# Kernel optimization log

Measured on AMD Instinct MI355X. Metric: run time of the kernel, lower is better.

Reference implementation:

```python
import jax, jax.numpy as jnp
import numpy as np

B, T, D, DH, DFF = 4, 2048, 1024, 1024, 4096


def setup_inputs() -> dict:
    key = jax.random.key(0)
    ks = jax.random.split(key, 8)
    s = 0.02
    return {
        "x": jax.random.normal(ks[0], (B, T, D), jnp.float32),
        "ln1_g": jnp.ones((D,), jnp.float32),
        "ln1_b": jnp.zeros((D,), jnp.float32),
        "W_q": jax.random.normal(ks[1], (D, DH), jnp.float32) * s,
        "b_q": jnp.zeros((DH,), jnp.float32),
        "W_k": jax.random.normal(ks[2], (D, DH), jnp.float32) * s,
        "b_k": jnp.zeros((DH,), jnp.float32),
        "W_v": jax.random.normal(ks[3], (D, DH), jnp.float32) * s,
        "b_v": jnp.zeros((DH,), jnp.float32),
        "ln2_g": jnp.ones((D,), jnp.float32),
        "ln2_b": jnp.zeros((D,), jnp.float32),
        "W_in": jax.random.normal(ks[4], (D, DFF), jnp.float32) * s,
        "b_in": jnp.zeros((DFF,), jnp.float32),
        "W_out": jax.random.normal(ks[5], (DFF, D), jnp.float32) * s,
        "b_out": jnp.zeros((D,), jnp.float32),
    }


def _layernorm(x, g, b, eps=1e-5):
    mu = jnp.mean(x, axis=-1, keepdims=True)
    var = jnp.var(x, axis=-1, keepdims=True)
    return (x - mu) * jax.lax.rsqrt(var + eps) * g + b


def reference(x, ln1_g, ln1_b, W_q, b_q, W_k, b_k, W_v, b_v,
              ln2_g, ln2_b, W_in, b_in, W_out, b_out):
    # --- attention branch (pre-LN) ---
    h = _layernorm(x, ln1_g, ln1_b)                      # [B,T,D]
    Q = h @ W_q + b_q                                    # [B,T,DH]
    K = h @ W_k + b_k
    V = h @ W_v + b_v
    scale = 1.0 / jnp.sqrt(jnp.asarray(K.shape[-1], h.dtype))
    att = jnp.einsum("btd,bsd->bts", Q, K) * scale       # [B,T,T]
    # NOTE: source calls att.masked_fill(...) without assignment -> mask
    # is discarded; faithfully no causal mask applied here.
    att = jax.nn.softmax(att, axis=-1)
    attn_out = jnp.einsum("bts,bsd->btd", att, V)        # [B,T,DH]
    x = x + attn_out
    # --- MLP branch (pre-LN) ---
    h2 = _layernorm(x, ln2_g, ln2_b)
    ff = jax.nn.gelu(h2 @ W_in + b_in, approximate=False)
    x = x + (ff @ W_out + b_out)
    return x
```

## Files before the change

### kernel.cpp

```cpp
#include <hip/hip_runtime.h>
#include <hip/hip_bf16.h>

#define B_    4
#define T_    2048
#define D_    1024
#define DH_   1024
#define DFF_  4096
#define MTOT  (B_ * T_)

using f32x4  = __attribute__((ext_vector_type(4))) float;
using bf16x8 = __attribute__((ext_vector_type(8))) short;

__device__ __forceinline__ unsigned short f2bf(float f) {
    unsigned u = __builtin_bit_cast(unsigned, f);
    u += 0x7fffu + ((u >> 16) & 1u);
    return (unsigned short)(u >> 16);
}
__device__ __forceinline__ float bf2f(unsigned short h) {
    unsigned u = ((unsigned)h) << 16;
    return __builtin_bit_cast(float, u);
}

__device__ __forceinline__ void gload16(const short* g, short* l) {
    __builtin_amdgcn_global_load_lds(
        (const __attribute__((address_space(1))) unsigned int*)g,
        (__attribute__((address_space(3))) unsigned int*)l, 16, 0, 0);
}

__global__ __launch_bounds__(256) void transp_f32_bf16(
    const float* __restrict__ src, short* __restrict__ dst, int K, int N) {
    __shared__ float tile[32][33];
    int tk = blockIdx.y * 32, tn = blockIdx.x * 32;
    int tx = threadIdx.x & 31, ty = threadIdx.x >> 5;
#pragma unroll
    for (int i = 0; i < 4; i++) {
        int r = ty + i * 8;
        tile[r][tx] = src[(size_t)(tk + r) * N + tn + tx];
    }
    __syncthreads();
#pragma unroll
    for (int i = 0; i < 4; i++) {
        int r = ty + i * 8;
        dst[(size_t)(tn + r) * K + tk + tx] = f2bf(tile[tx][r]);
    }
}

__global__ void copyv(const float* __restrict__ s, float* __restrict__ d, int n) {
    int i = blockIdx.x * blockDim.x + threadIdx.x;
    if (i < n) d[i] = s[i];
}

__global__ __launch_bounds__(256) void ln_rows(
    const float* __restrict__ x, const float* __restrict__ g,
    const float* __restrict__ bta, short* __restrict__ out) {
    int row = blockIdx.x;
    const float* xr = x + (size_t)row * D_;
    int t = threadIdx.x;
    float4 v = *(const float4*)(xr + t * 4);
    float s  = v.x + v.y + v.z + v.w;
    float s2 = v.x * v.x + v.y * v.y + v.z * v.z + v.w * v.w;
#pragma unroll
    for (int off = 1; off < 64; off <<= 1) {
        s  += __shfl_xor(s, off);
        s2 += __shfl_xor(s2, off);
    }
    __shared__ float as_[4], as2_[4];
    int wave = t >> 6, lane = t & 63;
    if (lane == 0) { as_[wave] = s; as2_[wave] = s2; }
    __syncthreads();
    s  = as_[0] + as_[1] + as_[2] + as_[3];
    s2 = as2_[0] + as2_[1] + as2_[2] + as2_[3];
    float mean = s * (1.0f / D_);
    float var  = s2 * (1.0f / D_) - mean * mean;
    float rstd = rsqrtf(var + 1e-5f);
    float4 gv = *(const float4*)(g + t * 4);
    float4 bv = *(const float4*)(bta + t * 4);
    short4 o;
    o.x = f2bf((v.x - mean) * rstd * gv.x + bv.x);
    o.y = f2bf((v.y - mean) * rstd * gv.y + bv.y);
    o.z = f2bf((v.z - mean) * rstd * gv.z + bv.z);
    o.w = f2bf((v.w - mean) * rstd * gv.w + bv.w);
    *(short4*)(out + (size_t)row * D_ + t * 4) = o;
}

template<int NB, int BIAS_MODE, int ACT, int RES, int OUT_BF16>
__global__ __launch_bounds__(512, 2) void gemmT(
    const short* __restrict__ A, int lda, long long sA,
    const short* __restrict__ Bt, int ldb, long long sB,
    void* __restrict__ C, int ldc, long long sC,
    const float* __restrict__ bias,
    const float* __restrict__ res, int ldr, long long sR,
    int K) {
    extern __shared__ short smem_[];
    short* shA = smem_;
    short* shB = smem_ + 49152;
    const int SB = 4096 * NB;

    int gx = gridDim.x, gy = gridDim.y;
    int n2d = gx * gy;
    int nwg = n2d * gridDim.z;
    int lid = blockIdx.x + gx * (blockIdx.y + gy * blockIdx.z);
    int q = nwg >> 3, rq = nwg & 7, xcd = lid & 7, i_ = lid >> 3;
    int nid = (xcd < rq ? xcd * (q + 1) : rq * (q + 1) + (xcd - rq) * q) + i_;
    int z = nid / n2d, r2d = nid % n2d;
    int sw = gy << 2;
    int strip = r2d / sw, rr = r2d % sw;
    int by = rr >> 2, bx = (strip << 2) + (rr & 3);

    int bm = by * 256, bn = bx * (64 * NB);
    const short* gA = A  + (size_t)z * sA + (size_t)bm * lda;
    const short* gB = Bt + (size_t)z * sB + (size_t)bn * ldb;
    int tid = threadIdx.x, lane = tid & 63, w = tid >> 6;
    int wr = w >> 2, wc = w & 3;

    int rbase = tid >> 3;
    int gcol  = ((((tid & 7) << 4) ^ ((rbase & 7) << 4)) >> 1);
    const short* pA[4]; const short* pB[4];
#pragma unroll
    for (int c = 0; c < 4; c++)
        pA[c] = gA + (size_t)(c * 64 + rbase) * lda + gcol;
#pragma unroll
    for (int c = 0; c < NB; c++)
        pB[c] = gB + (size_t)(c * 64 + rbase) * ldb + gcol;

    int aoff[8], boff[4];
#pragma unroll
    for (int f = 0; f < 8; f++) {
        int row = wr * 128 + f * 16 + (lane & 15);
        aoff[f] = row * 128 + ((((lane >> 4) * 16)) ^ ((row & 7) << 4));
    }
#pragma unroll
    for (int f = 0; f < NB; f++) {
        int row = wc * (16 * NB) + f * 16 + (lane & 15);
        boff[f] = row * 128 + ((((lane >> 4) * 16)) ^ ((row & 7) << 4));
    }

    int nk = K >> 6;
    f32x4 acc[8][NB] = {};

#define MFROW(r_, av) \
    _Pragma("unroll") \
    for (int n_ = 0; n_ < NB; n_++) \
        acc[r_][n_] = __builtin_amdgcn_mfma_f32_16x16x32_bf16(av, bfv[n_], acc[r_][n_], 0, 0, 0);

    if constexpr (NB == 4) {
        gload16(pA[0], shA + 0 * 4096 + tid * 8);
        gload16(pA[2], shA + 2 * 4096 + tid * 8);
        gload16(pA[1], shA + 1 * 4096 + tid * 8);
        gload16(pA[3], shA + 3 * 4096 + tid * 8);
        gload16(pB[0], shB + 0 * 4096 + tid * 8);
        gload16(pB[1], shB + 1 * 4096 + tid * 8);
        gload16(pB[2], shB + 2 * 4096 + tid * 8);
        gload16(pB[3], shB + 3 * 4096 + tid * 8);
        gload16(pA[0] + 64, shA + 16384 + 0 * 4096 + tid * 8);
        gload16(pA[2] + 64, shA + 16384 + 2 * 4096 + tid * 8);
        gload16(pA[1] + 64, shA + 16384 + 1 * 4096 + tid * 8);
        gload16(pA[3] + 64, shA + 16384 + 3 * 4096 + tid * 8);
        gload16(pB[0] + 64, shB + 16384 + 0 * 4096 + tid * 8);
        gload16(pB[1] + 64, shB + 16384 + 1 * 4096 + tid * 8);
        asm volatile("s_waitcnt vmcnt(6)" ::: "memory");
        __builtin_amdgcn_s_barrier();

        for (int t = 0; t < nk; t++) {
            const char* sA_ = (const char*)(shA + (t % 3) * 16384);
            const char* sB_ = (const char*)(shB + (t & 1) * 16384);
            short* wA2 = shA + ((t + 2) % 3) * 16384;
            short* wB1 = shB + ((t + 1) & 1) * 16384;
            short* wB2 = shB + (t & 1) * 16384;
            int ka  = (t + 2 < nk ? t + 2 : nk - 1) << 6;
            int kb1 = (t + 1 < nk ? t + 1 : nk - 1) << 6;
            bf16x8 af[4], bfv[4];

#pragma unroll
            for (int f = 0; f < 4; f++) af[f] = *(const bf16x8*)(sA_ + aoff[f]);
#pragma unroll
            for (int f = 0; f < 4; f++) bfv[f] = *(const bf16x8*)(sB_ + boff[f]);
            gload16(pB[2] + kb1, wB1 + 2 * 4096 + tid * 8);
            gload16(pB[3] + kb1, wB1 + 3 * 4096 + tid * 8);
            __builtin_amdgcn_s_barrier();
            asm volatile("s_waitcnt lgkmcnt(0)" ::: "memory");
            __builtin_amdgcn_s_setprio(1);
            MFROW(0, af[0]) MFROW(1, af[1]) MFROW(2, af[2]) MFROW(3, af[3])
            __builtin_amdgcn_s_setprio(0);
            __builtin_amdgcn_s_barrier();
#pragma unroll
            for (int f = 0; f < 4; f++) af[f] = *(const bf16x8*)(sA_ + aoff[4 + f]);
            gload16(pA[0] + ka, wA2 + 0 * 4096 + tid * 8);
            gload16(pA[2] + ka, wA2 + 2 * 4096 + tid * 8);
            __builtin_amdgcn_s_barrier();
            asm volatile("s_waitcnt lgkmcnt(0)" ::: "memory");
            __builtin_amdgcn_s_setprio(1);
            MFROW(4, af[0]) MFROW(5, af[1]) MFROW(6, af[2]) MFROW(7, af[3])
            __builtin_amdgcn_s_setprio(0);
            __builtin_amdgcn_s_barrier();
#pragma unroll
            for (int f = 0; f < 4; f++) af[f] = *(const bf16x8*)(sA_ + (aoff[f] ^ 64));
#pragma unroll
            for (int f = 0; f < 4; f++) bfv[f] = *(const bf16x8*)(sB_ + (boff[f] ^ 64));
            gload16(pA[1] + ka, wA2 + 1 * 4096 + tid * 8);
            gload16(pA[3] + ka, wA2 + 3 * 4096 + tid * 8);
            __builtin_amdgcn_s_barrier();
            asm volatile("s_waitcnt lgkmcnt(0)" ::: "memory");
            __builtin_amdgcn_s_setprio(1);
            MFROW(0, af[0]) MFROW(1, af[1]) MFROW(2, af[2]) MFROW(3, af[3])
            __builtin_amdgcn_s_setprio(0);
            __builtin_amdgcn_s_barrier();
#pragma unroll
            for (int f = 0; f < 4; f++) af[f] = *(const bf16x8*)(sA_ + (aoff[4 + f] ^ 64));
            gload16(pB[0] + ka, wB2 + 0 * 4096 + tid * 8);
            gload16(pB[1] + ka, wB2 + 1 * 4096 + tid * 8);
            __builtin_amdgcn_s_barrier();
            asm volatile("s_waitcnt lgkmcnt(0)" ::: "memory");
            __builtin_amdgcn_s_setprio(1);
            MFROW(4, af[0]) MFROW(5, af[1]) MFROW(6, af[2]) MFROW(7, af[3])
            __builtin_amdgcn_s_setprio(0);
            asm volatile("s_waitcnt vmcnt(6)" ::: "memory");
            __builtin_amdgcn_s_barrier();
        }
    } else {
#pragma unroll
        for (int s = 0; s < 2; s++) {
#pragma unroll
            for (int c = 0; c < 4; c++)
                gload16(pA[c] + s * 64, shA + s * 16384 + c * 4096 + tid * 8);
#pragma unroll
            for (int c = 0; c < 2; c++)
                gload16(pB[c] + s * 64, shB + s * 8192 + c * 4096 + tid * 8);
        }
        asm volatile("s_waitcnt vmcnt(6)" ::: "memory");
        __builtin_amdgcn_s_barrier();

        for (int t = 0; t < nk; t++) {
            int rs = t % 3, es = (t + 2) % 3;
            const char* sA_ = (const char*)(shA + rs * 16384);
            const char* sB_ = (const char*)(shB + rs * 8192);
            short* wA = shA + es * 16384;
            short* wB = shB + es * 8192;
            int ks = (t + 2 < nk ? t + 2 : nk - 1) << 6;
            bf16x8 af[8], bfv[2];

#pragma unroll
            for (int f = 0; f < 8; f++) af[f] = *(const bf16x8*)(sA_ + aoff[f]);
#pragma unroll
            for (int f = 0; f < 2; f++) bfv[f] = *(const bf16x8*)(sB_ + boff[f]);
            gload16(pA[0] + ks, wA + tid * 8);
            gload16(pA[1] + ks, wA + 4096 + tid * 8);
            gload16(pA[2] + ks, wA + 2 * 4096 + tid * 8);
            gload16(pA[3] + ks, wA + 3 * 4096 + tid * 8);
            gload16(pB[0] + ks, wB + tid * 8);
            gload16(pB[1] + ks, wB + 4096 + tid * 8);
            __builtin_amdgcn_s_barrier();
            asm volatile("s_waitcnt lgkmcnt(0)" ::: "memory");
            __builtin_amdgcn_s_setprio(1);
            MFROW(0, af[0]) MFROW(1, af[1]) MFROW(2, af[2]) MFROW(3, af[3])
            MFROW(4, af[4]) MFROW(5, af[5]) MFROW(6, af[6]) MFROW(7, af[7])
            __builtin_amdgcn_s_setprio(0);
            __builtin_amdgcn_s_barrier();
#pragma unroll
            for (int f = 0; f < 8; f++) af[f] = *(const bf16x8*)(sA_ + (aoff[f] ^ 64));
#pragma unroll
            for (int f = 0; f < 2; f++) bfv[f] = *(const bf16x8*)(sB_ + (boff[f] ^ 64));
            __builtin_amdgcn_s_barrier();
            asm volatile("s_waitcnt lgkmcnt(0)" ::: "memory");
            __builtin_amdgcn_s_setprio(1);
            MFROW(0, af[0]) MFROW(1, af[1]) MFROW(2, af[2]) MFROW(3, af[3])
            MFROW(4, af[4]) MFROW(5, af[5]) MFROW(6, af[6]) MFROW(7, af[7])
            __builtin_amdgcn_s_setprio(0);
            asm volatile("s_waitcnt vmcnt(6)" ::: "memory");
            __builtin_amdgcn_s_barrier();
        }
    }
#undef MFROW
    asm volatile("s_waitcnt vmcnt(0)" ::: "memory");

    size_t zc = (size_t)z * (size_t)sC;
    float* lpart = (float*)smem_;
#pragma unroll
    for (int fr = 0; fr < 8; fr++) {
        float pr[4] = {0.f, 0.f, 0.f, 0.f};
        float s8[4];
        if (RES == 2) {
#pragma unroll
            for (int r_ = 0; r_ < 4; r_++) {
                int row = bm + wr * 128 + fr * 16 + (lane >> 4) * 4 + r_;
                float s = 0.f;
#pragma unroll
                for (int i = 0; i < 8; i++) s += bias[((size_t)z * 8 + i) * 2048 + row];
                s8[r_] = 1.0f / s;
            }
        }
#pragma unroll
        for (int fn = 0; fn < NB; fn++) {
            int colc = bn + wc * (16 * NB) + fn * 16 + (lane & 15);
#pragma unroll
            for (int r_ = 0; r_ < 4; r_++) {
                int row = bm + wr * 128 + fr * 16 + (lane >> 4) * 4 + r_;
                float v = acc[fr][fn][r_];
                if (BIAS_MODE == 1) v += bias[colc];
                else if (BIAS_MODE == 2) v += bias[row];
                if (ACT == 1) v = 0.5f * v * (1.0f + erff(v * 0.70710678118654752f));
                if (ACT == 2) {
                    v = expf(v * 0.03125f);
                    unsigned short us = f2bf(v);
                    ((short*)C)[zc + (size_t)row * ldc + colc] = (short)us;
                    pr[r_] += bf2f(us);
                    continue;
                }
                if (RES == 1) v += res[(size_t)z * sR + (size_t)row * ldr + colc];
                if (RES == 2) v = v * s8[r_] + res[(size_t)z * sR + (size_t)row * ldr + colc];
                if (OUT_BF16) ((short*)C)[zc + (size_t)row * ldc + colc] = f2bf(v);
                else          ((float*)C)[zc + (size_t)row * ldc + colc] = v;
            }
        }
        if (ACT == 2) {
#pragma unroll
            for (int m_ = 1; m_ < 16; m_ <<= 1) {
#pragma unroll
                for (int r_ = 0; r_ < 4; r_++) pr[r_] += __shfl_xor(pr[r_], m_);
            }
            if ((lane & 15) == 0) {
#pragma unroll
                for (int r_ = 0; r_ < 4; r_++)
                    lpart[wc * 256 + wr * 128 + fr * 16 + (lane >> 4) * 4 + r_] = pr[r_];
            }
        }
    }
    if (ACT == 2) {
        __syncthreads();
        if (tid < 256) {
            float s = lpart[tid] + lpart[256 + tid] + lpart[512 + tid] + lpart[768 + tid];
            ((float*)res)[((size_t)z * 8 + bx) * 2048 + bm + tid] = s;
        }
    }
}

#define SHB4 163840
#define SHB2 147456

extern "C" void kernel_launch(void* const* d_in, const int* in_sizes, int n_in,
                              void* d_out, int out_size, void* d_ws, size_t ws_size,
                              hipStream_t stream) {
    const float* x    = (const float*)d_in[0];
    const float* ln1g = (const float*)d_in[1];
    const float* ln1b = (const float*)d_in[2];
    const float* Wq   = (const float*)d_in[3];
    const float* bq   = (const float*)d_in[4];
    const float* Wk   = (const float*)d_in[5];
    const float* bk   = (const float*)d_in[6];
    const float* Wv   = (const float*)d_in[7];
    const float* bv   = (const float*)d_in[8];
    const float* ln2g = (const float*)d_in[9];
    const float* ln2b = (const float*)d_in[10];
    const float* Win  = (const float*)d_in[11];
    const float* bin  = (const float*)d_in[12];
    const float* Wout = (const float*)d_in[13];
    const float* bout = (const float*)d_in[14];

    char* ws = (char*)d_ws;
    size_t off = 0;
    auto alloc = [&](size_t bytes) {
        void* p = ws + off;
        off += (bytes + 255) & ~(size_t)255;
        return p;
    };
    short* WqkT  = (short*)alloc((size_t)2048 * 1024 * 2);
    short* WvT   = (short*)alloc((size_t)1024 * 1024 * 2);
    short* WinT  = (short*)alloc((size_t)4096 * 1024 * 2);
    short* WoutT = (short*)alloc((size_t)1024 * 4096 * 2);
    float* bqk   = (float*)alloc((size_t)2048 * 4);
    short* h     = (short*)alloc((size_t)MTOT * 1024 * 2);
    short* QK    = (short*)alloc((size_t)MTOT * 2048 * 2);
    short* VT    = (short*)alloc((size_t)1024 * 8192 * 2);
    float* S     = (float*)alloc((size_t)4 * 2048 * 2048 * 4);
    float* x1    = (float*)alloc((size_t)MTOT * 1024 * 4);
    float* rowsums = (float*)alloc((size_t)4 * 8 * 2048 * 4);
    (void)ws_size; (void)in_sizes; (void)n_in; (void)out_size;

    hipFuncSetAttribute((const void*)gemmT<4,1,0,0,1>, hipFuncAttributeMaxDynamicSharedMemorySize, SHB4);
    hipFuncSetAttribute((const void*)gemmT<4,0,2,0,1>, hipFuncAttributeMaxDynamicSharedMemorySize, SHB4);
    hipFuncSetAttribute((const void*)gemmT<4,1,1,0,1>, hipFuncAttributeMaxDynamicSharedMemorySize, SHB4);
    hipFuncSetAttribute((const void*)gemmT<2,2,0,0,1>, hipFuncAttributeMaxDynamicSharedMemorySize, SHB2);
    hipFuncSetAttribute((const void*)gemmT<2,0,0,2,0>, hipFuncAttributeMaxDynamicSharedMemorySize, SHB2);
    hipFuncSetAttribute((const void*)gemmT<2,1,0,1,0>, hipFuncAttributeMaxDynamicSharedMemorySize, SHB2);

    transp_f32_bf16<<<dim3(32, 32), 256, 0, stream>>>(Wq, WqkT, 1024, 1024);
    transp_f32_bf16<<<dim3(32, 32), 256, 0, stream>>>(Wk, WqkT + (size_t)1024 * 1024, 1024, 1024);
    transp_f32_bf16<<<dim3(32, 32), 256, 0, stream>>>(Wv, WvT, 1024, 1024);
    transp_f32_bf16<<<dim3(128, 32), 256, 0, stream>>>(Win, WinT, 1024, 4096);
    transp_f32_bf16<<<dim3(32, 128), 256, 0, stream>>>(Wout, WoutT, 4096, 1024);
    copyv<<<4, 256, 0, stream>>>(bq, bqk, 1024);
    copyv<<<4, 256, 0, stream>>>(bk, bqk + 1024, 1024);

    ln_rows<<<MTOT, 256, 0, stream>>>(x, ln1g, ln1b, h);

    gemmT<4, 1, 0, 0, 1><<<dim3(8, 32, 1), 512, SHB4, stream>>>(
        h, 1024, 0, WqkT, 1024, 0, QK, 2048, 0, bqk, nullptr, 0, 0, 1024);

    gemmT<2, 2, 0, 0, 1><<<dim3(64, 4, 1), 512, SHB2, stream>>>(
        WvT, 1024, 0, h, 1024, 0, VT, 8192, 0, bv, nullptr, 0, 0, 1024);

    gemmT<4, 0, 2, 0, 1><<<dim3(8, 8, 4), 512, SHB4, stream>>>(
        QK, 2048, 4194304LL, QK + 1024, 2048, 4194304LL,
        (short*)S, 4096, 8388608LL, nullptr, (const float*)rowsums, 0, 0, 1024);

    gemmT<2, 0, 0, 2, 0><<<dim3(8, 8, 4), 512, SHB2, stream>>>(
        (short*)S, 4096, 8388608LL, VT, 8192, 2048LL,
        x1, 1024, 2097152LL, rowsums, x, 1024, 2097152LL, 2048);

    ln_rows<<<MTOT, 256, 0, stream>>>(x1, ln2g, ln2b, h);

    short* ff = (short*)S;
    gemmT<4, 1, 1, 0, 1><<<dim3(16, 32, 1), 512, SHB4, stream>>>(
        h, 1024, 0, WinT, 1024, 0, ff, 4096, 0, bin, nullptr, 0, 0, 1024);

    gemmT<2, 1, 0, 1, 0><<<dim3(8, 32, 1), 512, SHB2, stream>>>(
        ff, 4096, 0, WoutT, 4096, 0, (float*)d_out, 1024, 0, bout,
        x1, 1024, 0, 4096);
}
```

Baseline: 391.3 us.

## Software-pipeline LDS fragment reads with double-buffered registers in GEMM main loop

```diff
diff --git a/kernel.cpp b/kernel.cpp
--- a/kernel.cpp
+++ b/kernel.cpp
@@ -94,7 +94,6 @@
     extern __shared__ short smem_[];
     short* shA = smem_;
     short* shB = smem_ + 49152;
-    const int SB = 4096 * NB;
 
     int gx = gridDim.x, gy = gridDim.y;
     int n2d = gx * gy;
@@ -137,11 +136,6 @@
 
     int nk = K >> 6;
     f32x4 acc[8][NB] = {};
-
-#define MFROW(r_, av) \
-    _Pragma("unroll") \
-    for (int n_ = 0; n_ < NB; n_++) \
-        acc[r_][n_] = __builtin_amdgcn_mfma_f32_16x16x32_bf16(av, bfv[n_], acc[r_][n_], 0, 0, 0);
 
     if constexpr (NB == 4) {
         gload16(pA[0], shA + 0 * 4096 + tid * 8);
@@ -161,62 +155,81 @@
         asm volatile("s_waitcnt vmcnt(6)" ::: "memory");
         __builtin_amdgcn_s_barrier();
 
+        bf16x8 aA[4], aB[4], b0[4], b1[4];
+        {
+            const char* s0A = (const char*)shA;
+            const char* s0B = (const char*)shB;
+#pragma unroll
+            for (int f = 0; f < 4; f++) aA[f] = *(const bf16x8*)(s0A + aoff[f]);
+#pragma unroll
+            for (int f = 0; f < 4; f++) b0[f] = *(const bf16x8*)(s0B + boff[f]);
+            asm volatile("s_waitcnt lgkmcnt(0)" ::: "memory");
+        }
+
+#define MF4(r_, av, bv) \
+        acc[r_][0] = __builtin_amdgcn_mfma_f32_16x16x32_bf16(av, bv[0], acc[r_][0], 0, 0, 0); \
+        acc[r_][1] = __builtin_amdgcn_mfma_f32_16x16x32_bf16(av, bv[1], acc[r_][1], 0, 0, 0); \
+        acc[r_][2] = __builtin_amdgcn_mfma_f32_16x16x32_bf16(av, bv[2], acc[r_][2], 0, 0, 0); \
+        acc[r_][3] = __builtin_amdgcn_mfma_f32_16x16x32_bf16(av, bv[3], acc[r_][3], 0, 0, 0);
+
         for (int t = 0; t < nk; t++) {
-            const char* sA_ = (const char*)(shA + (t % 3) * 16384);
-            const char* sB_ = (const char*)(shB + (t & 1) * 16384);
+            const char* sA_  = (const char*)(shA + (t % 3) * 16384);
+            const char* sB_  = (const char*)(shB + (t & 1) * 16384);
+            const char* sA1_ = (const char*)(shA + ((t + 1) % 3) * 16384);
+            const char* sB1_ = (const char*)(shB + ((t + 1) & 1) * 16384);
             short* wA2 = shA + ((t + 2) % 3) * 16384;
             short* wB1 = shB + ((t + 1) & 1) * 16384;
             short* wB2 = shB + (t & 1) * 16384;
             int ka  = (t + 2 < nk ? t + 2 : nk - 1) << 6;
             int kb1 = (t + 1 < nk ? t + 1 : nk - 1) << 6;
-            bf16x8 af[4], bfv[4];
-
-#pragma unroll
-            for (int f = 0; f < 4; f++) af[f] = *(const bf16x8*)(sA_ + aoff[f]);
-#pragma unroll
-            for (int f = 0; f < 4; f++) bfv[f] = *(const bf16x8*)(sB_ + boff[f]);
+
+#pragma unroll
+            for (int f = 0; f < 4; f++) aB[f] = *(const bf16x8*)(sA_ + aoff[4 + f]);
             gload16(pB[2] + kb1, wB1 + 2 * 4096 + tid * 8);
             gload16(pB[3] + kb1, wB1 + 3 * 4096 + tid * 8);
-            __builtin_amdgcn_s_barrier();
-            asm volatile("s_waitcnt lgkmcnt(0)" ::: "memory");
-            __builtin_amdgcn_s_setprio(1);
-            MFROW(0, af[0]) MFROW(1, af[1]) MFROW(2, af[2]) MFROW(3, af[3])
-            __builtin_amdgcn_s_setprio(0);
-            __builtin_amdgcn_s_barrier();
-#pragma unroll
-            for (int f = 0; f < 4; f++) af[f] = *(const bf16x8*)(sA_ + aoff[4 + f]);
+            asm volatile("s_waitcnt lgkmcnt(4)" ::: "memory");
+            __builtin_amdgcn_sched_barrier(0);
+            __builtin_amdgcn_s_setprio(1);
+            MF4(0, aA[0], b0) MF4(1, aA[1], b0) MF4(2, aA[2], b0) MF4(3, aA[3], b0)
+            __builtin_amdgcn_s_setprio(0);
+            __builtin_amdgcn_s_barrier();
+#pragma unroll
+            for (int f = 0; f < 4; f++) aA[f] = *(const bf16x8*)(sA_ + (aoff[f] ^ 64));
+#pragma unroll
+            for (int f = 0; f < 4; f++) b1[f] = *(const bf16x8*)(sB_ + (boff[f] ^ 64));
             gload16(pA[0] + ka, wA2 + 0 * 4096 + tid * 8);
             gload16(pA[2] + ka, wA2 + 2 * 4096 + tid * 8);
-            __builtin_amdgcn_s_barrier();
-            asm volatile("s_waitcnt lgkmcnt(0)" ::: "memory");
-            __builtin_amdgcn_s_setprio(1);
-            MFROW(4, af[0]) MFROW(5, af[1]) MFROW(6, af[2]) MFROW(7, af[3])
-            __builtin_amdgcn_s_setprio(0);
-            __builtin_amdgcn_s_barrier();
-#pragma unroll
-            for (int f = 0; f < 4; f++) af[f] = *(const bf16x8*)(sA_ + (aoff[f] ^ 64));
-#pragma unroll
-            for (int f = 0; f < 4; f++) bfv[f] = *(const bf16x8*)(sB_ + (boff[f] ^ 64));
+            asm volatile("s_waitcnt lgkmcnt(8)" ::: "memory");
+            __builtin_amdgcn_sched_barrier(0);
+            __builtin_amdgcn_s_setprio(1);
+            MF4(4, aB[0], b0) MF4(5, aB[1], b0) MF4(6, aB[2], b0) MF4(7, aB[3], b0)
+            __builtin_amdgcn_s_setprio(0);
+            __builtin_amdgcn_s_barrier();
+#pragma unroll
+            for (int f = 0; f < 4; f++) aB[f] = *(const bf16x8*)(sA_ + (aoff[4 + f] ^ 64));
             gload16(pA[1] + ka, wA2 + 1 * 4096 + tid * 8);
             gload16(pA[3] + ka, wA2 + 3 * 4096 + tid * 8);
-            __builtin_amdgcn_s_barrier();
-            asm volatile("s_waitcnt lgkmcnt(0)" ::: "memory");
-            __builtin_amdgcn_s_setprio(1);
-            MFROW(0, af[0]) MFROW(1, af[1]) MFROW(2, af[2]) MFROW(3, af[3])
-            __builtin_amdgcn_s_setprio(0);
-            __builtin_amdgcn_s_barrier();
-#pragma unroll
-            for (int f = 0; f < 4; f++) af[f] = *(const bf16x8*)(sA_ + (aoff[4 + f] ^ 64));
+            asm volatile("s_waitcnt lgkmcnt(4)" ::: "memory");
+            __builtin_amdgcn_sched_barrier(0);
+            __builtin_amdgcn_s_setprio(1);
+            MF4(0, aA[0], b1) MF4(1, aA[1], b1) MF4(2, aA[2], b1) MF4(3, aA[3], b1)
+            __builtin_amdgcn_s_setprio(0);
+            asm volatile("s_waitcnt vmcnt(4)" ::: "memory");
+            __builtin_amdgcn_s_barrier();
+#pragma unroll
+            for (int f = 0; f < 4; f++) aA[f] = *(const bf16x8*)(sA1_ + aoff[f]);
+#pragma unroll
+            for (int f = 0; f < 4; f++) b0[f] = *(const bf16x8*)(sB1_ + boff[f]);
             gload16(pB[0] + ka, wB2 + 0 * 4096 + tid * 8);
             gload16(pB[1] + ka, wB2 + 1 * 4096 + tid * 8);
-            __builtin_amdgcn_s_barrier();
-            asm volatile("s_waitcnt lgkmcnt(0)" ::: "memory");
-            __builtin_amdgcn_s_setprio(1);
-            MFROW(4, af[0]) MFROW(5, af[1]) MFROW(6, af[2]) MFROW(7, af[3])
-            __builtin_amdgcn_s_setprio(0);
-            asm volatile("s_waitcnt vmcnt(6)" ::: "memory");
-            __builtin_amdgcn_s_barrier();
-        }
+            asm volatile("s_waitcnt lgkmcnt(8)" ::: "memory");
+            __builtin_amdgcn_sched_barrier(0);
+            __builtin_amdgcn_s_setprio(1);
+            MF4(4, aB[0], b1) MF4(5, aB[1], b1) MF4(6, aB[2], b1) MF4(7, aB[3], b1)
+            __builtin_amdgcn_s_setprio(0);
+            __builtin_amdgcn_s_barrier();
+        }
+#undef MF4
     } else {
 #pragma unroll
         for (int s = 0; s < 2; s++) {
@@ -230,48 +243,64 @@
         asm volatile("s_waitcnt vmcnt(6)" ::: "memory");
         __builtin_amdgcn_s_barrier();
 
+        bf16x8 aA[8], aB[8], b0[2], b1[2];
+        {
+            const char* s0A = (const char*)shA;
+            const char* s0B = (const char*)shB;
+#pragma unroll
+            for (int f = 0; f < 8; f++) aA[f] = *(const bf16x8*)(s0A + aoff[f]);
+#pragma unroll
+            for (int f = 0; f < 2; f++) b0[f] = *(const bf16x8*)(s0B + boff[f]);
+            asm volatile("s_waitcnt lgkmcnt(0)" ::: "memory");
+        }
+
+#define MF2(r_, av, bv) \
+        acc[r_][0] = __builtin_amdgcn_mfma_f32_16x16x32_bf16(av, bv[0], acc[r_][0], 0, 0, 0); \
+        acc[r_][1] = __builtin_amdgcn_mfma_f32_16x16x32_bf16(av, bv[1], acc[r_][1], 0, 0, 0);
+
         for (int t = 0; t < nk; t++) {
-            int rs = t % 3, es = (t + 2) % 3;
-            const char* sA_ = (const char*)(shA + rs * 16384);
-            const char* sB_ = (const char*)(shB + rs * 8192);
-            short* wA = shA + es * 16384;
-            short* wB = shB + es * 8192;
+            const char* sA_  = (const char*)(shA + (t % 3) * 16384);
+            const char* sB_  = (const char*)(shB + (t % 3) * 8192);
+            const char* sA1_ = (const char*)(shA + ((t + 1) % 3) * 16384);
+            const char* sB1_ = (const char*)(shB + ((t + 1) % 3) * 8192);
+            short* wA = shA + ((t + 2) % 3) * 16384;
+            short* wB = shB + ((t + 2) % 3) * 8192;
             int ks = (t + 2 < nk ? t + 2 : nk - 1) << 6;
-            bf16x8 af[8], bfv[2];
-
-#pragma unroll
-            for (int f = 0; f < 8; f++) af[f] = *(const bf16x8*)(sA_ + aoff[f]);
-#pragma unroll
-            for (int f = 0; f < 2; f++) bfv[f] = *(const bf16x8*)(sB_ + boff[f]);
+
+#pragma unroll
+            for (int f = 0; f < 8; f++) aB[f] = *(const bf16x8*)(sA_ + (aoff[f] ^ 64));
+#pragma unroll
+            for (int f = 0; f < 2; f++) b1[f] = *(const bf16x8*)(sB_ + (boff[f] ^ 64));
             gload16(pA[0] + ks, wA + tid * 8);
             gload16(pA[1] + ks, wA + 4096 + tid * 8);
             gload16(pA[2] + ks, wA + 2 * 4096 + tid * 8);
             gload16(pA[3] + ks, wA + 3 * 4096 + tid * 8);
             gload16(pB[0] + ks, wB + tid * 8);
             gload16(pB[1] + ks, wB + 4096 + tid * 8);
-            __builtin_amdgcn_s_barrier();
-            asm volatile("s_waitcnt lgkmcnt(0)" ::: "memory");
-            __builtin_amdgcn_s_setprio(1);
-            MFROW(0, af[0]) MFROW(1, af[1]) MFROW(2, af[2]) MFROW(3, af[3])
-            MFROW(4, af[4]) MFROW(5, af[5]) MFROW(6, af[6]) MFROW(7, af[7])
-            __builtin_amdgcn_s_setprio(0);
-            __builtin_amdgcn_s_barrier();
-#pragma unroll
-            for (int f = 0; f < 8; f++) af[f] = *(const bf16x8*)(sA_ + (aoff[f] ^ 64));
-#pragma unroll
-            for (int f = 0; f < 2; f++) bfv[f] = *(const bf16x8*)(sB_ + (boff[f] ^ 64));
-            __builtin_amdgcn_s_barrier();
-            asm volatile("s_waitcnt lgkmcnt(0)" ::: "memory");
-            __builtin_amdgcn_s_setprio(1);
-            MFROW(0, af[0]) MFROW(1, af[1]) MFROW(2, af[2]) MFROW(3, af[3])
-            MFROW(4, af[4]) MFROW(5, af[5]) MFROW(6, af[6]) MFROW(7, af[7])
+            asm volatile("s_waitcnt lgkmcnt(10)" ::: "memory");
+            __builtin_amdgcn_sched_barrier(0);
+            __builtin_amdgcn_s_setprio(1);
+            MF2(0, aA[0], b0) MF2(1, aA[1], b0) MF2(2, aA[2], b0) MF2(3, aA[3], b0)
+            MF2(4, aA[4], b0) MF2(5, aA[5], b0) MF2(6, aA[6], b0) MF2(7, aA[7], b0)
             __builtin_amdgcn_s_setprio(0);
             asm volatile("s_waitcnt vmcnt(6)" ::: "memory");
             __builtin_amdgcn_s_barrier();
-        }
-    }
-#undef MFROW
+#pragma unroll
+            for (int f = 0; f < 8; f++) aA[f] = *(const bf16x8*)(sA1_ + aoff[f]);
+#pragma unroll
+            for (int f = 0; f < 2; f++) b0[f] = *(const bf16x8*)(sB1_ + boff[f]);
+            asm volatile("s_waitcnt lgkmcnt(10)" ::: "memory");
+            __builtin_amdgcn_sched_barrier(0);
+            __builtin_amdgcn_s_setprio(1);
+            MF2(0, aB[0], b1) MF2(1, aB[1], b1) MF2(2, aB[2], b1) MF2(3, aB[3], b1)
+            MF2(4, aB[4], b1) MF2(5, aB[5], b1) MF2(6, aB[6], b1) MF2(7, aB[7], b1)
+            __builtin_amdgcn_s_setprio(0);
+            __builtin_amdgcn_s_barrier();
+        }
+#undef MF2
+    }
     asm volatile("s_waitcnt vmcnt(0)" ::: "memory");
+    __syncthreads();
 
     size_t zc = (size_t)z * (size_t)sC;
     float* lpart = (float*)smem_;
```

New measurement: 382.9 us. -2.1%, faster.
